# Kernel optimization log

Hardware: AMD Instinct MI355X
Metric: run time of the kernel (lower is better)

## Reference

```python
import jax, jax.numpy as jnp
import numpy as np

N = 50000        # n nodes (cells)
C = 1024         # common genes
H = 128          # edge_h_dim
HG = 128         # edge_hidden
E = 1600000      # edges (avg degree 32)
LAYERS = 2       # gnn_layers (unset in original __init__; fixed here)
EPS = 1e-8


def setup_inputs() -> dict:
    key = jax.random.key(0)
    ks = jax.random.split(key, 10)
    x_common = jax.random.normal(ks[0], (N, C), dtype=jnp.float32)
    src = jax.random.randint(ks[1], (E,), 0, N, dtype=jnp.int32)
    dst = jax.random.randint(ks[2], (E,), 0, N, dtype=jnp.int32)
    base_w = jax.random.uniform(ks[3], (E,), dtype=jnp.float32)
    # encoder params: Linear(C,H) -> ReLU -> Linear(H,H) -> ReLU
    W1 = jax.random.normal(ks[4], (C, H), dtype=jnp.float32) * 0.02
    b1 = jnp.zeros((H,), dtype=jnp.float32)
    W2 = jax.random.normal(ks[5], (H, H), dtype=jnp.float32) * 0.1
    b2 = jnp.zeros((H,), dtype=jnp.float32)
    # edge gate params: Linear(2H, HG) -> ReLU -> Linear(HG, 1)
    Wg1 = jax.random.normal(ks[6], (2 * H, HG), dtype=jnp.float32) * 0.1
    bg1 = jnp.zeros((HG,), dtype=jnp.float32)
    Wg2 = jax.random.normal(ks[7], (HG, 1), dtype=jnp.float32) * 0.1
    bg2 = jnp.full((1,), 2.0, dtype=jnp.float32)  # original init: bias=2.0
    # node reliability logits
    rho_raw = jax.random.normal(ks[8], (N,), dtype=jnp.float32) * 0.5
    return dict(x_common=x_common, src=src, dst=dst, base_w=base_w,
                W1=W1, b1=b1, W2=W2, b2=b2,
                Wg1=Wg1, bg1=bg1, Wg2=Wg2, bg2=bg2, rho_raw=rho_raw)


def reference(x_common, src, dst, base_w, W1, b1, W2, b2, Wg1, bg1, Wg2, bg2, rho_raw):
    # enc: [N, C] -> [N, H]
    h = jax.nn.relu(jax.nn.relu(x_common @ W1 + b1) @ W2 + b2)
    rho = jax.nn.sigmoid(rho_raw)                 # [N]
    rr = rho[src] * rho[dst]                      # [E] per-edge reliability factor
    for _ in range(LAYERS):
        h_src = h[src]                            # [E, H] gather
        h_dst = h[dst]                            # [E, H] gather
        z = jnp.concatenate([h_src, h_dst], axis=1)               # [E, 2H]
        gate = jax.nn.sigmoid(jax.nn.relu(z @ Wg1 + bg1) @ Wg2 + bg2)[:, 0]  # [E]
        w = base_w * gate * rr                    # [E]
        m = jax.ops.segment_sum(w[:, None] * h_src, dst, num_segments=N)     # [N, H]
        deg = jax.ops.segment_sum(w, dst, num_segments=N)                    # [N]
        h = m / (deg[:, None] + EPS)
    return h
```

## Files before the change

kernel.cpp:

```cpp
#include <hip/hip_runtime.h>
#include <stdint.h>

#define NN 50000
#define CC 1024
#define HH 128
#define EE 1600000
#define EPSV 1e-8f
#define SCAN_BLKS 196

typedef __attribute__((ext_vector_type(8))) short bf16x8;
typedef __attribute__((ext_vector_type(4))) float f32x4;
typedef __attribute__((ext_vector_type(2))) float f32x2;

__device__ __forceinline__ unsigned short f32_to_bf16(float f){
  union { float f; uint32_t u; } cv; cv.f = f;
  uint32_t u = cv.u;
  return (unsigned short)((u + 0x7FFFu + ((u >> 16) & 1u)) >> 16);
}
__device__ __forceinline__ float bf16lo_to_f32(uint32_t w){
  union { uint32_t u; float f; } cv; cv.u = w << 16; return cv.f;
}
__device__ __forceinline__ float bf16hi_to_f32(uint32_t w){
  union { uint32_t u; float f; } cv; cv.u = w & 0xFFFF0000u; return cv.f;
}

#define DPP_ADD(x, ctrl) ((x) + __int_as_float(__builtin_amdgcn_update_dpp(0, __float_as_int(x), (ctrl), 0xF, 0xF, true)))

#define GLOAD_LDS16(g, l) __builtin_amdgcn_global_load_lds( \
    (const __attribute__((address_space(1))) uint32_t*)(g), \
    (__attribute__((address_space(3))) uint32_t*)(l), 16, 0, 0)


__global__ __launch_bounds__(256) void k_prep_all(
    const float* __restrict__ W1, const float* __restrict__ W2,
    const float* __restrict__ Wg1,
    unsigned short* __restrict__ W1T, unsigned short* __restrict__ W2T,
    unsigned short* __restrict__ Wg1T){
  int idx = blockIdx.x*256 + threadIdx.x;
  if(idx < 131072){
    int n = idx >> 10, k = idx & 1023;
    W1T[idx] = f32_to_bf16(W1[k*128 + n]);
  } else if(idx < 131072 + 16384){
    int i = idx - 131072;
    int n = i >> 7, k = i & 127;
    W2T[i] = f32_to_bf16(W2[k*128 + n]);
  } else if(idx < 131072 + 16384 + 32768){
    int i = idx - 131072 - 16384;
    int c = i >> 7, k = i & 127;
    int row = (c < 128) ? k : (128 + k);
    int col = (c < 128) ? c : (c - 128);
    Wg1T[i] = f32_to_bf16(Wg1[row*128 + col]);
  }
}


__global__ __launch_bounds__(256) void k_hist(const int* __restrict__ dst,
                                              int* __restrict__ counts,
                                              int* __restrict__ rank){
  int e = blockIdx.x*256 + threadIdx.x;
  if(e < EE) rank[e] = atomicAdd(&counts[dst[e]], 1);
}

__global__ __launch_bounds__(256) void k_scan1(const int* __restrict__ counts,
    int* __restrict__ lexcl, int* __restrict__ bsum){
  __shared__ int buf[256];
  const int t = threadIdx.x, i = blockIdx.x*256 + t;
  int v = (i < NN) ? counts[i] : 0;
  buf[t] = v;
  __syncthreads();
  for(int off = 1; off < 256; off <<= 1){
    int add = (t >= off) ? buf[t-off] : 0;
    __syncthreads();
    buf[t] += add;
    __syncthreads();
  }
  if(i < NN) lexcl[i] = buf[t] - v;
  if(t == 255) bsum[blockIdx.x] = buf[255];
}

__global__ __launch_bounds__(256) void k_scan2(const int* __restrict__ bsum,
    int* __restrict__ bexcl, int* __restrict__ row_ptr){
  __shared__ int buf[256];
  const int t = threadIdx.x;
  int v = (t < SCAN_BLKS) ? bsum[t] : 0;
  buf[t] = v;
  __syncthreads();
  for(int off = 1; off < 256; off <<= 1){
    int add = (t >= off) ? buf[t-off] : 0;
    __syncthreads();
    buf[t] += add;
    __syncthreads();
  }
  if(t < SCAN_BLKS) bexcl[t] = buf[t] - v;
  if(t == 255) row_ptr[NN] = buf[255];
}

__global__ __launch_bounds__(256) void k_scan3(const int* __restrict__ lexcl,
    const int* __restrict__ bexcl, int* __restrict__ row_ptr){
  const int i = blockIdx.x*256 + threadIdx.x;
  if(i >= NN) return;
  row_ptr[i] = lexcl[i] + bexcl[blockIdx.x];
}

__global__ __launch_bounds__(256) void k_fill(const int* __restrict__ src,
    const int* __restrict__ dst, const float* __restrict__ base_w,
    const float* __restrict__ rho_raw, const int* __restrict__ row_ptr,
    const int* __restrict__ rank, float2* __restrict__ scp){
  int e = blockIdx.x*256 + threadIdx.x;
  if(e >= EE) return;
  int s = src[e], d = dst[e];
  int p = row_ptr[d] + rank[e];
  float rs = 1.f/(1.f + __expf(-rho_raw[s]));
  float rd = 1.f/(1.f + __expf(-rho_raw[d]));
  scp[p] = make_float2(base_w[e]*rs*rd, __int_as_float(s));
}


__global__ __launch_bounds__(256) void k_enc1(
    const float* __restrict__ X, const unsigned short* __restrict__ W1T,
    const float* __restrict__ b1, unsigned short* __restrict__ h1)
{
  __shared__ __attribute__((aligned(16))) float          Af[2][32*32];
  __shared__ __attribute__((aligned(16))) unsigned short Bf[2][128*32];

  const int t = threadIdx.x, w = t >> 6, lane = t & 63;
  const int rowL = lane & 15, kq = lane >> 4;
  const int wm = w >> 1, wn = w & 1;
  const int row0 = blockIdx.x * 32;

  const int a_rl = w*8 + (lane >> 3);
  const int a_cl = lane & 7;
  int agr = row0 + a_rl; if(agr >= NN) agr = NN-1;
  const float* a_src = X + (size_t)agr*1024 + (a_cl ^ (a_rl & 7))*4;
  const int b_rl0 = w*32 + (lane >> 2);
  const int b_cl  = lane & 3;
  const int bkey0 = (b_rl0 ^ (b_rl0 >> 2)) & 3;
  const int bkey1 = ((b_rl0+16) ^ ((b_rl0+16) >> 2)) & 3;
  const unsigned short* b_src0 = W1T + (size_t)b_rl0*1024 + (b_cl ^ bkey0)*8;
  const unsigned short* b_src1 = W1T + (size_t)(b_rl0+16)*1024 + (b_cl ^ bkey1)*8;

  #define STAGE(buf, k0)  do{                                              \
    GLOAD_LDS16(a_src  + (k0), &Af[buf][(w*8)*32]);                        \
    GLOAD_LDS16(b_src0 + (k0), &Bf[buf][(w*32     )*32]);                  \
    GLOAD_LDS16(b_src1 + (k0), &Bf[buf][(w*32 + 16)*32]);                  \
  }while(0)

  STAGE(0, 0);
  __syncthreads();

  f32x4 acc[4] = {};
  const int arow  = wm*16 + rowL;
  const int akey  = rowL & 7;
  const int bkeyR = (rowL ^ (rowL >> 2)) & 3;

  int cur = 0;
  for(int step = 0; step < 32; step++){
    if(step < 31) STAGE(cur^1, (step+1)*32);
    f32x4 x0 = *(const f32x4*)&Af[cur][arow*32 + (((2*kq  ) ^ akey) << 2)];
    f32x4 x1 = *(const f32x4*)&Af[cur][arow*32 + (((2*kq+1) ^ akey) << 2)];
    union { bf16x8 v; unsigned short s[8]; } pk;
    #pragma unroll
    for(int j = 0; j < 4; j++){ pk.s[j] = f32_to_bf16(x0[j]); pk.s[4+j] = f32_to_bf16(x1[j]); }
    bf16x8 bfr[4];
    #pragma unroll
    for(int nf = 0; nf < 4; nf++){
      const int br = wn*64 + nf*16 + rowL;
      bfr[nf] = *(const bf16x8*)&Bf[cur][br*32 + ((kq ^ bkeyR) << 3)];
    }
    #pragma unroll
    for(int nf = 0; nf < 4; nf++)
      acc[nf] = __builtin_amdgcn_mfma_f32_16x16x32_bf16(pk.v, bfr[nf], acc[nf], 0, 0, 0);
    __syncthreads();
    cur ^= 1;
  }
  #undef STAGE

  #pragma unroll
  for(int nf = 0; nf < 4; nf++){
    const int col = wn*64 + nf*16 + rowL;
    const float bv = b1[col];
    #pragma unroll
    for(int r = 0; r < 4; r++){
      const int gr = row0 + wm*16 + kq*4 + r;
      if(gr < NN) h1[(size_t)gr*128 + col] = f32_to_bf16(fmaxf(acc[nf][r] + bv, 0.f));
    }
  }
}


__device__ __forceinline__ void uv_phase2(
    const unsigned short* hs, const unsigned short* wgl, int row0, int wave, int lane,
    const float* __restrict__ bg1,
    unsigned short* __restrict__ UH, float* __restrict__ Vf)
{
  const int rowL = lane & 15, kq = lane >> 4;
  const int r = wave*16 + rowL;
  f32x4 acc[16] = {};
  #pragma unroll
  for(int ks = 0; ks < 4; ks++){
    const int kc = ks*4 + kq;
    bf16x8 a = *(const bf16x8*)&hs[r*128 + ((kc ^ (r & 15)) << 3)];
    #pragma unroll
    for(int nt = 0; nt < 16; nt++){
      bf16x8 b = *(const bf16x8*)&wgl[(nt*16 + rowL)*128 + ((kc ^ rowL) << 3)];
      acc[nt] = __builtin_amdgcn_mfma_f32_16x16x32_bf16(a, b, acc[nt], 0, 0, 0);
    }
  }
  #pragma unroll
  for(int nt = 0; nt < 16; nt++){
    const int col = nt*16 + rowL;
    #pragma unroll
    for(int rr = 0; rr < 4; rr++){
      const int gr = row0 + wave*16 + kq*4 + rr;
      if(gr < NN){
        if(col < 128) UH[(size_t)gr*256 + col] = f32_to_bf16(acc[nt][rr]);
        else          Vf[(size_t)gr*128 + col - 128] = acc[nt][rr] + bg1[col - 128];
      }
    }
  }
}


__global__ __launch_bounds__(256) void k_uvA(
    const unsigned short* __restrict__ h1, const unsigned short* __restrict__ W2T,
    const float* __restrict__ b2, const unsigned short* __restrict__ Wg1T,
    const float* __restrict__ bg1, unsigned short* __restrict__ UH,
    float* __restrict__ Vf)
{
  __shared__ __attribute__((aligned(16))) unsigned short hs[64*128];
  __shared__ __attribute__((aligned(16))) unsigned short wgl[256*128];
  const int t = threadIdx.x, wave = t >> 6, lane = t & 63;
  const int rowL = lane & 15, kq = lane >> 4;
  const int row0 = blockIdx.x*64;

  bf16x8 wreg[16];
  #pragma unroll
  for(int i = 0; i < 16; i++)
    wreg[i] = *(const bf16x8*)(Wg1T + (i*256 + t)*8);

  int ar = row0 + wave*16 + rowL; if(ar >= NN) ar = NN-1;
  f32x4 acc[8] = {};
  #pragma unroll
  for(int ks = 0; ks < 4; ks++){
    bf16x8 a = *(const bf16x8*)(h1 + (size_t)ar*128 + ks*32 + kq*8);
    #pragma unroll
    for(int nt = 0; nt < 8; nt++){
      bf16x8 b = *(const bf16x8*)(W2T + (nt*16 + rowL)*128 + ks*32 + kq*8);
      acc[nt] = __builtin_amdgcn_mfma_f32_16x16x32_bf16(a, b, acc[nt], 0, 0, 0);
    }
  }
  #pragma unroll
  for(int nt = 0; nt < 8; nt++){
    const int col = nt*16 + rowL;
    const float bv = b2[col];
    #pragma unroll
    for(int r = 0; r < 4; r++){
      const int rw = wave*16 + kq*4 + r;
      const unsigned short hv = f32_to_bf16(fmaxf(acc[nt][r] + bv, 0.f));
      hs[rw*128 + (((col >> 3) ^ (rw & 15)) << 3) + (col & 7)] = hv;
    }
  }
  #pragma unroll
  for(int i = 0; i < 16; i++){
    const int idx = i*256 + t, row = idx >> 4, c = idx & 15;
    *(bf16x8*)&wgl[row*128 + ((c ^ (row & 15)) << 3)] = wreg[i];
  }
  __syncthreads();
  {
    const int r = t >> 2, gr = row0 + r;
    if(gr < NN){
      #pragma unroll
      for(int j8 = 0; j8 < 4; j8++){
        const int chunk = (t & 3)*4 + j8;
        bf16x8 v = *(const bf16x8*)&hs[r*128 + ((chunk ^ (r & 15)) << 3)];
        *(bf16x8*)&UH[(size_t)gr*256 + 128 + chunk*8] = v;
      }
    }
  }
  uv_phase2(hs, wgl, row0, wave, lane, bg1, UH, Vf);
}


__global__ __launch_bounds__(256) void k_uvB(
    const float* __restrict__ hf, const unsigned short* __restrict__ Wg1T,
    const float* __restrict__ bg1, unsigned short* __restrict__ UH,
    float* __restrict__ Vf)
{
  __shared__ __attribute__((aligned(16))) unsigned short hs[64*128];
  __shared__ __attribute__((aligned(16))) unsigned short wgl[256*128];
  const int t = threadIdx.x, wave = t >> 6, lane = t & 63;
  const int row0 = blockIdx.x*64;

  bf16x8 wreg[16];
  #pragma unroll
  for(int i = 0; i < 16; i++)
    wreg[i] = *(const bf16x8*)(Wg1T + (i*256 + t)*8);

  {
    const int r = t >> 2, gr0 = row0 + r;
    const int gr = (gr0 < NN) ? gr0 : NN-1;
    const float* p = hf + (size_t)gr*128 + (t & 3)*32;
    #pragma unroll
    for(int j8 = 0; j8 < 4; j8++){
      f32x4 v0 = *(const f32x4*)(p + j8*8);
      f32x4 v1 = *(const f32x4*)(p + j8*8 + 4);
      union { bf16x8 v; unsigned short s[8]; } pk;
      #pragma unroll
      for(int j = 0; j < 4; j++){ pk.s[j] = f32_to_bf16(v0[j]); pk.s[4+j] = f32_to_bf16(v1[j]); }
      const int chunk = (t & 3)*4 + j8;
      *(bf16x8*)&hs[r*128 + ((chunk ^ (r & 15)) << 3)] = pk.v;
      if(gr0 < NN) *(bf16x8*)&UH[(size_t)gr0*256 + 128 + chunk*8] = pk.v;
    }
  }
  #pragma unroll
  for(int i = 0; i < 16; i++){
    const int idx = i*256 + t, row = idx >> 4, c = idx & 15;
    *(bf16x8*)&wgl[row*128 + ((c ^ (row & 15)) << 3)] = wreg[i];
  }
  __syncthreads();
  uv_phase2(hs, wgl, row0, wave, lane & 63, bg1, UH, Vf);
}


__global__ __launch_bounds__(256) void k_gate_agg(
    const unsigned short* __restrict__ UH, const float* __restrict__ Vf,
    const int* __restrict__ row_ptr, const float2* __restrict__ scp,
    const float* __restrict__ Wg2, const float* __restrict__ bg2p,
    float* __restrict__ out_f32)
{
  __shared__ float2 ws_s[4][64];
  const int wv = threadIdx.x >> 6, lane = threadIdx.x & 63;
  const int gw = blockIdx.x*4 + wv;
  if(gw >= NN) return;
  const int eq = lane >> 4, li = lane & 15;

  f32x4 va = *(const f32x4*)(Vf + (size_t)gw*128 + li*8);
  f32x4 vb = *(const f32x4*)(Vf + (size_t)gw*128 + li*8 + 4);
  f32x4 wa = *(const f32x4*)(Wg2 + li*8);
  f32x4 wb = *(const f32x4*)(Wg2 + li*8 + 4);
  const float vch[8]  = {va[0],va[1],va[2],va[3],vb[0],vb[1],vb[2],vb[3]};
  const float w2ch[8] = {wa[0],wa[1],wa[2],wa[3],wb[0],wb[1],wb[2],wb[3]};
  const float bg2v = bg2p[0];

  const int beg = row_ptr[gw], end = row_ptr[gw+1];
  float a0 = 0.f, a1 = 0.f, wsum = 0.f;

  for(int base = beg; base < end; base += 64){
    const int nb = min(64, end - base);

    float2 sc_c0, sc_c1; bf16x8 u_c0, u_c1;
    {
      const int i0 = (eq     < nb) ? eq     : 0;
      const int i1 = (4 + eq < nb) ? 4 + eq : 0;
      sc_c0 = scp[base + i0]; sc_c1 = scp[base + i1];
      u_c0 = *(const bf16x8*)&UH[(uint32_t)__float_as_int(sc_c0.y)*256u + li*8];
      u_c1 = *(const bf16x8*)&UH[(uint32_t)__float_as_int(sc_c1.y)*256u + li*8];
    }
    for(int q = 0; q < nb; q += 8){
      float2 sc_n0 = sc_c0, sc_n1 = sc_c1; bf16x8 u_n0 = u_c0, u_n1 = u_c1;
      if(q + 8 < nb){
        const int i0 = (q + 8  + eq < nb) ? q + 8  + eq : 0;
        const int i1 = (q + 12 + eq < nb) ? q + 12 + eq : 0;
        sc_n0 = scp[base + i0]; sc_n1 = scp[base + i1];
        u_n0 = *(const bf16x8*)&UH[(uint32_t)__float_as_int(sc_n0.y)*256u + li*8];
        u_n1 = *(const bf16x8*)&UH[(uint32_t)__float_as_int(sc_n1.y)*256u + li*8];
      }
      {
        union { bf16x8 v; uint32_t u32[4]; } uu; uu.v = u_c0;
        float tacc = 0.f;
        #pragma unroll
        for(int p = 0; p < 4; p++){
          const uint32_t w2b = uu.u32[p];
          tacc += fmaxf(bf16lo_to_f32(w2b) + vch[2*p],   0.f) * w2ch[2*p];
          tacc += fmaxf(bf16hi_to_f32(w2b) + vch[2*p+1], 0.f) * w2ch[2*p+1];
        }
        tacc = DPP_ADD(tacc, 0xB1);
        tacc = DPP_ADD(tacc, 0x4E);
        tacc = DPP_ADD(tacc, 0x141);
        tacc = DPP_ADD(tacc, 0x140);
        const float g = 1.f/(1.f + __expf(-(tacc + bg2v)));
        const int idx = q + eq;
        if(li == 0 && idx < nb) ws_s[wv][idx] = make_float2(sc_c0.x*g, sc_c0.y);
      }
      {
        union { bf16x8 v; uint32_t u32[4]; } uu; uu.v = u_c1;
        float tacc = 0.f;
        #pragma unroll
        for(int p = 0; p < 4; p++){
          const uint32_t w2b = uu.u32[p];
          tacc += fmaxf(bf16lo_to_f32(w2b) + vch[2*p],   0.f) * w2ch[2*p];
          tacc += fmaxf(bf16hi_to_f32(w2b) + vch[2*p+1], 0.f) * w2ch[2*p+1];
        }
        tacc = DPP_ADD(tacc, 0xB1);
        tacc = DPP_ADD(tacc, 0x4E);
        tacc = DPP_ADD(tacc, 0x141);
        tacc = DPP_ADD(tacc, 0x140);
        const float g = 1.f/(1.f + __expf(-(tacc + bg2v)));
        const int idx = q + 4 + eq;
        if(li == 0 && idx < nb) ws_s[wv][idx] = make_float2(sc_c1.x*g, sc_c1.y);
      }
      sc_c0 = sc_n0; sc_c1 = sc_n1; u_c0 = u_n0; u_c1 = u_n1;
    }

    #pragma unroll 8
    for(int j = 0; j < nb; j++){
      const float2 p = ws_s[wv][j];
      const float w  = p.x;
      const uint32_t s = (uint32_t)__float_as_int(p.y);
      const uint32_t hw = *(const uint32_t*)&UH[s*256u + 128u + lane*2];
      a0 += w*bf16lo_to_f32(hw);
      a1 += w*bf16hi_to_f32(hw);
      wsum += w;
    }
  }
  const float inv = 1.f/(wsum + EPSV);
  const size_t o = (size_t)gw*128 + lane*2;
  *(f32x2*)&out_f32[o] = (f32x2){a0*inv, a1*inv};
}


extern "C" void kernel_launch(void* const* d_in, const int* in_sizes, int n_in,
                              void* d_out, int out_size, void* d_ws, size_t ws_size,
                              hipStream_t stream) {
  (void)in_sizes; (void)n_in; (void)out_size; (void)ws_size;
  const float* X      = (const float*)d_in[0];
  const int*   src    = (const int*)d_in[1];
  const int*   dst    = (const int*)d_in[2];
  const float* base_w = (const float*)d_in[3];
  const float* W1     = (const float*)d_in[4];
  const float* b1     = (const float*)d_in[5];
  const float* W2     = (const float*)d_in[6];
  const float* b2     = (const float*)d_in[7];
  const float* Wg1    = (const float*)d_in[8];
  const float* bg1    = (const float*)d_in[9];
  const float* Wg2    = (const float*)d_in[10];
  const float* bg2    = (const float*)d_in[11];
  const float* rho    = (const float*)d_in[12];

  char* ws = (char*)d_ws;
  size_t off = 0;
  auto alloc = [&](size_t bytes)->char*{ char* p = ws + off; off += (bytes + 255) & ~(size_t)255; return p; };
  unsigned short* W1T      = (unsigned short*)alloc((size_t)1024*128*2);
  unsigned short* W2T      = (unsigned short*)alloc((size_t)128*128*2);
  unsigned short* Wg1T     = (unsigned short*)alloc((size_t)256*128*2);
  int*            rank     = (int*)alloc((size_t)EE*4);
  float2*         scp      = (float2*)alloc((size_t)EE*8);
  int*            row_ptr  = (int*)alloc((size_t)(NN+1)*4);
  int*            counts   = (int*)alloc((size_t)NN*4);
  int*            lexcl    = (int*)alloc((size_t)NN*4);
  int*            bsum     = (int*)alloc((size_t)256*4);
  int*            bexcl    = (int*)alloc((size_t)256*4);
  unsigned short* h1       = (unsigned short*)alloc((size_t)NN*128*2);
  unsigned short* UH       = (unsigned short*)alloc((size_t)NN*256*2);
  float*          Vf       = (float*)alloc((size_t)NN*128*4);
  float*          hf_B     = (float*)alloc((size_t)NN*128*4);

  hipMemsetAsync(counts, 0, (size_t)NN*4, stream);
  k_prep_all<<<704, 256, 0, stream>>>(W1, W2, Wg1, W1T, W2T, Wg1T);
  k_hist<<<EE/256, 256, 0, stream>>>(dst, counts, rank);
  k_scan1<<<SCAN_BLKS, 256, 0, stream>>>(counts, lexcl, bsum);
  k_scan2<<<1, 256, 0, stream>>>(bsum, bexcl, row_ptr);
  k_scan3<<<SCAN_BLKS, 256, 0, stream>>>(lexcl, bexcl, row_ptr);
  k_fill<<<EE/256, 256, 0, stream>>>(src, dst, base_w, rho, row_ptr, rank, scp);

  k_enc1<<<1563, 256, 0, stream>>>(X, W1T, b1, h1);

  k_uvA<<<782, 256, 0, stream>>>(h1, W2T, b2, Wg1T, bg1, UH, Vf);
  k_gate_agg<<<12500, 256, 0, stream>>>(UH, Vf, row_ptr, scp, Wg2, bg2, hf_B);
  k_uvB<<<782, 256, 0, stream>>>(hf_B, Wg1T, bg1, UH, Vf);
  k_gate_agg<<<12500, 256, 0, stream>>>(UH, Vf, row_ptr, scp, Wg2, bg2, (float*)d_out);
}
```

Baseline: 510.6 us.

## Triple-buffer encoder GEMM loads with explicit vmcnt waits

Converts the first encoder layer's double-buffered LDS pipeline into a triple-buffered one, issuing global-to-LDS loads two k-steps ahead. Explicit s_waitcnt vmcnt counts and raw barriers replace __syncthreads so that loads for later stages can stay outstanding while the current tile is computed. This is meant to hide global memory latency on the X stream, at the cost of 50% more LDS per block and possible lower occupancy.

```diff
diff --git a/kernel.cpp b/kernel.cpp
--- a/kernel.cpp
+++ b/kernel.cpp
@@ -120,8 +120,8 @@
     const float* __restrict__ X, const unsigned short* __restrict__ W1T,
     const float* __restrict__ b1, unsigned short* __restrict__ h1)
 {
-  __shared__ __attribute__((aligned(16))) float          Af[2][32*32];
-  __shared__ __attribute__((aligned(16))) unsigned short Bf[2][128*32];
+  __shared__ __attribute__((aligned(16))) float          Af[3][32*32];
+  __shared__ __attribute__((aligned(16))) unsigned short Bf[3][128*32];
 
   const int t = threadIdx.x, w = t >> 6, lane = t & 63;
   const int rowL = lane & 15, kq = lane >> 4;
@@ -145,19 +145,14 @@
     GLOAD_LDS16(b_src1 + (k0), &Bf[buf][(w*32 + 16)*32]);                  \
   }while(0)
 
-  STAGE(0, 0);
-  __syncthreads();
-
   f32x4 acc[4] = {};
   const int arow  = wm*16 + rowL;
   const int akey  = rowL & 7;
   const int bkeyR = (rowL ^ (rowL >> 2)) & 3;
 
-  int cur = 0;
-  for(int step = 0; step < 32; step++){
-    if(step < 31) STAGE(cur^1, (step+1)*32);
-    f32x4 x0 = *(const f32x4*)&Af[cur][arow*32 + (((2*kq  ) ^ akey) << 2)];
-    f32x4 x1 = *(const f32x4*)&Af[cur][arow*32 + (((2*kq+1) ^ akey) << 2)];
+  auto COMPUTE = [&](const float* afb, const unsigned short* bfb){
+    f32x4 x0 = *(const f32x4*)&afb[arow*32 + (((2*kq  ) ^ akey) << 2)];
+    f32x4 x1 = *(const f32x4*)&afb[arow*32 + (((2*kq+1) ^ akey) << 2)];
     union { bf16x8 v; unsigned short s[8]; } pk;
     #pragma unroll
     for(int j = 0; j < 4; j++){ pk.s[j] = f32_to_bf16(x0[j]); pk.s[4+j] = f32_to_bf16(x1[j]); }
@@ -165,14 +160,36 @@
     #pragma unroll
     for(int nf = 0; nf < 4; nf++){
       const int br = wn*64 + nf*16 + rowL;
-      bfr[nf] = *(const bf16x8*)&Bf[cur][br*32 + ((kq ^ bkeyR) << 3)];
+      bfr[nf] = *(const bf16x8*)&bfb[br*32 + ((kq ^ bkeyR) << 3)];
     }
     #pragma unroll
     for(int nf = 0; nf < 4; nf++)
       acc[nf] = __builtin_amdgcn_mfma_f32_16x16x32_bf16(pk.v, bfr[nf], acc[nf], 0, 0, 0);
-    __syncthreads();
-    cur ^= 1;
-  }
+  };
+
+  #define STEP(cbuf, sbuf, sk, vN)  do{                                    \
+    if((sk) >= 0) STAGE(sbuf, (sk)*32);                                    \
+    asm volatile("s_waitcnt vmcnt(" #vN ")" ::: "memory");                 \
+    __builtin_amdgcn_s_barrier();                                          \
+    __builtin_amdgcn_sched_barrier(0);                                     \
+    COMPUTE(&Af[cbuf][0], &Bf[cbuf][0]);                                   \
+    __builtin_amdgcn_s_barrier();                                          \
+  }while(0)
+
+  STAGE(0, 0);
+  STAGE(1, 32);
+
+  for(int tt = 0; tt < 30; tt += 3){
+    STEP(0, 2, tt + 2, 6);
+    STEP(1, 0, tt + 3, 6);
+    STEP(2, 1, tt + 4, 6);
+  }
+  STEP(0, 0, -1, 3);
+  asm volatile("s_waitcnt vmcnt(0)" ::: "memory");
+  __builtin_amdgcn_s_barrier();
+  __builtin_amdgcn_sched_barrier(0);
+  COMPUTE(&Af[1][0], &Bf[1][0]);
+  #undef STEP
   #undef STAGE
 
   #pragma unroll
```

Result: no change. 511.3 us (+0.1%).
